# Optimization experiments

Measured on AMD Instinct MI355X. Metric: run time of the kernel, lower is better.

Reference implementation:

```python
import jax, jax.numpy as jnp
import numpy as np

N_NODES = 50000
N_EDGES = 800000
IN_CH = 128
HID = 128
N_GRAPHS = 512


def setup_inputs() -> dict:
    key = jax.random.key(0)
    ks = jax.random.split(key, 12)
    x = jax.random.normal(ks[0], (N_NODES, IN_CH), dtype=jnp.float32)
    edge_index = jax.random.randint(ks[1], (2, N_EDGES), 0, N_NODES, dtype=jnp.int64)
    batch = jnp.sort(jax.random.randint(ks[2], (N_NODES,), 0, N_GRAPHS, dtype=jnp.int64))
    s = 0.05
    params = {
        'W1l': jax.random.normal(ks[3], (HID, IN_CH), dtype=jnp.float32) * s,
        'W1r': jax.random.normal(ks[4], (HID, IN_CH), dtype=jnp.float32) * s,
        'b1': jax.random.normal(ks[5], (HID,), dtype=jnp.float32) * s,
        'W2l': jax.random.normal(ks[6], (HID, HID), dtype=jnp.float32) * s,
        'W2r': jax.random.normal(ks[7], (HID, HID), dtype=jnp.float32) * s,
        'b2': jax.random.normal(ks[8], (HID,), dtype=jnp.float32) * s,
        'W3l': jax.random.normal(ks[9], (HID, HID), dtype=jnp.float32) * s,
        'W3r': jax.random.normal(ks[10], (HID, HID), dtype=jnp.float32) * s,
        'b3': jax.random.normal(ks[11], (HID,), dtype=jnp.float32) * s,
    }
    return {'x': x, 'edge_index': edge_index, 'batch': batch, **params}


def reference(x, edge_index, batch, W1l, W1r, b1, W2l, W2r, b2, W3l, W3r, b3):
    src = edge_index[0]
    dst = edge_index[1]
    n = x.shape[0]
    # in-degree for mean aggregation (nodes with no in-edges get 0 aggregate)
    deg = jax.ops.segment_sum(jnp.ones((src.shape[0],), x.dtype), dst, num_segments=n)
    inv_deg = (1.0 / jnp.maximum(deg, 1.0))[:, None]  # [N,1]

    def sage(h, Wl, Wr, b):
        # gather neighbor feats, scatter-mean to targets, then linear + root term
        agg = jax.ops.segment_sum(h[src], dst, num_segments=n) * inv_deg  # [N,d]
        return agg @ Wl.T + h @ Wr.T + b

    h = jax.nn.relu(sage(x, W1l, W1r, b1))
    h = jax.nn.relu(sage(h, W2l, W2r, b2))
    h = jax.nn.relu(sage(h, W3l, W3r, b3))

    # global mean pool over graph ids
    counts = jax.ops.segment_sum(jnp.ones((n,), h.dtype), batch, num_segments=N_GRAPHS)
    pooled = jax.ops.segment_sum(h, batch, num_segments=N_GRAPHS)
    return pooled / jnp.maximum(counts, 1.0)[:, None]
```

## Files before the change

kernel.cpp:

```cpp
#include <hip/hip_runtime.h>

#define N_NODES 50000
#define NP 50048
#define N_EDGES 800000
#define N_GRAPHS 512
#define F 128
#define ELLW 64

#define CASTX_BLOCKS 3128
#define CASTW_BLOCKS 48
#define ZERO_BLOCKS 49

typedef __bf16 bf16x8 __attribute__((ext_vector_type(8)));
typedef float f32x4 __attribute__((ext_vector_type(4)));
typedef unsigned short ushort_t;
typedef unsigned int uint_t;

__device__ inline ushort_t f2bf(float f) {
    uint_t u = __float_as_uint(f);
    u += 0x7FFFu + ((u >> 16) & 1u);
    return (ushort_t)(u >> 16);
}
__device__ inline float bf2f(ushort_t u) {
    return __uint_as_float(((uint_t)u) << 16);
}
__device__ inline uint_t pack2(float a, float b) {
    return (uint_t)f2bf(a) | ((uint_t)f2bf(b) << 16);
}

__global__ __launch_bounds__(256) void k_prep(
    const float* __restrict__ x,
    const float* __restrict__ w0, const float* __restrict__ w1,
    const float* __restrict__ w2, const float* __restrict__ w3,
    const float* __restrict__ w4, const float* __restrict__ w5,
    ushort_t* __restrict__ X, ushort_t* __restrict__ WB,
    int* __restrict__ cnt) {
    int b = blockIdx.x;
    int t = threadIdx.x;
    if (b < CASTX_BLOCKS) {
        int i = (b * 256 + t) * 8;
        uint4 o = make_uint4(0, 0, 0, 0);
        if (i < N_NODES * F) {
            float4 v0 = *(const float4*)&x[i];
            float4 v1 = *(const float4*)&x[i + 4];
            o = make_uint4(pack2(v0.x, v0.y), pack2(v0.z, v0.w),
                           pack2(v1.x, v1.y), pack2(v1.z, v1.w));
        }
        *(uint4*)&X[i] = o;
    } else if (b < CASTX_BLOCKS + CASTW_BLOCKS) {
        int idx = (b - CASTX_BLOCKS) * 256 + t;
        int m = idx >> 11;
        int o = (idx & 2047) * 8;
        const float* src = w0;
        if (m == 1) src = w1; else if (m == 2) src = w2; else if (m == 3) src = w3;
        else if (m == 4) src = w4; else if (m == 5) src = w5;
        float4 v0 = *(const float4*)&src[o];
        float4 v1 = *(const float4*)&src[o + 4];
        *(uint4*)&WB[m * 16384 + o] =
            make_uint4(pack2(v0.x, v0.y), pack2(v0.z, v0.w),
                       pack2(v1.x, v1.y), pack2(v1.z, v1.w));
    } else {
        int i = ((b - CASTX_BLOCKS - CASTW_BLOCKS) * 256 + t) * 4;
        *(int4*)&cnt[i] = make_int4(0, 0, 0, 0);
    }
}

__global__ __launch_bounds__(256) void k_fillell(const int* __restrict__ src,
                                                 const int* __restrict__ dst,
                                                 int* __restrict__ cnt,
                                                 int* __restrict__ ell) {
    int e = blockIdx.x * 256 + threadIdx.x;
    if (e < N_EDGES) {
        int d = dst[e];
        int pos = atomicAdd(&cnt[d], 1);
        if (pos < ELLW) ell[(d << 6) + pos] = src[e];
    }
}

__device__ inline void addrow(float* a, uint4 v) {
    a[0] += __uint_as_float(v.x << 16); a[1] += __uint_as_float(v.x & 0xFFFF0000u);
    a[2] += __uint_as_float(v.y << 16); a[3] += __uint_as_float(v.y & 0xFFFF0000u);
    a[4] += __uint_as_float(v.z << 16); a[5] += __uint_as_float(v.z & 0xFFFF0000u);
    a[6] += __uint_as_float(v.w << 16); a[7] += __uint_as_float(v.w & 0xFFFF0000u);
}

__global__ __launch_bounds__(256) void k_gather(const ushort_t* __restrict__ h,
                                                const int* __restrict__ ell,
                                                const int* __restrict__ cnt,
                                                ushort_t* __restrict__ agg) {
    int t = blockIdx.x * 256 + threadIdx.x;
    int n = t >> 4;
    int lane = t & 15;
    if (n >= N_NODES) return;
    int deg = min(cnt[n], ELLW);
    const int* el = ell + (n << 6);
    const uint4* h4 = (const uint4*)h;
    float ax[8], ay[8];
#pragma unroll
    for (int j = 0; j < 8; j++) { ax[j] = 0.f; ay[j] = 0.f; }
    int i = 0;
    for (; i + 4 <= deg; i += 4) {
        int s0 = el[i], s1 = el[i + 1], s2 = el[i + 2], s3 = el[i + 3];
        uint4 v0 = h4[(size_t)s0 * 16 + lane];
        uint4 v1 = h4[(size_t)s1 * 16 + lane];
        uint4 v2 = h4[(size_t)s2 * 16 + lane];
        uint4 v3 = h4[(size_t)s3 * 16 + lane];
        addrow(ax, v0); addrow(ay, v1); addrow(ax, v2); addrow(ay, v3);
    }
    for (; i < deg; i++) {
        uint4 v0 = h4[(size_t)el[i] * 16 + lane];
        addrow(ax, v0);
    }
    float sc = 1.0f / fmaxf((float)deg, 1.0f);
    uint_t r[4];
#pragma unroll
    for (int j = 0; j < 4; j++)
        r[j] = pack2((ax[2 * j] + ay[2 * j]) * sc,
                     (ax[2 * j + 1] + ay[2 * j + 1]) * sc);
    ((uint4*)agg)[(size_t)n * 16 + lane] = make_uint4(r[0], r[1], r[2], r[3]);
}

__global__ __launch_bounds__(256) void k_linear(const ushort_t* __restrict__ agg,
                                                const ushort_t* h,
                                                const ushort_t* __restrict__ Wl,
                                                const ushort_t* __restrict__ Wr,
                                                const float* __restrict__ bias,
                                                ushort_t* out) {
    __shared__ uint4 Alds4[512];
    __shared__ uint4 Blds4[1024];
    ushort_t* Alds = (ushort_t*)Alds4;
    ushort_t* Blds = (ushort_t*)Blds4;

    int t = threadIdx.x;
    int w = t >> 6;
    int lane = t & 63;
    int bm = blockIdx.x * 64;
    int wm = (w & 1) * 32;
    int wn = (w >> 1) * 64;
    int lrow = lane & 15;
    int kg = lane >> 4;

    f32x4 acc[2][4];
#pragma unroll
    for (int i = 0; i < 2; i++)
#pragma unroll
        for (int j = 0; j < 4; j++) acc[i][j] = (f32x4){0.f, 0.f, 0.f, 0.f};

    for (int iter = 0; iter < 4; iter++) {
        int kk = iter * 64;
        const ushort_t* A = (kk < 128) ? agg : h;
        const ushort_t* W = (kk < 128) ? Wl : Wr;
        int k0 = kk & 127;

        __syncthreads();
#pragma unroll
        for (int p = 0; p < 2; p++) {
            int chunkA = p * 4 + w;
            const ushort_t* gA = A + (size_t)(bm + lane) * F + k0 + chunkA * 8;
            ushort_t* lA = Alds + (size_t)(chunkA * 64) * 8;
            __builtin_amdgcn_global_load_lds(
                (const __attribute__((address_space(1))) void*)gA,
                (__attribute__((address_space(3))) void*)lA, 16, 0, 0);
        }
#pragma unroll
        for (int p = 0; p < 4; p++) {
            int chunkB = p * 2 + (w >> 1);
            int rbase = (w & 1) * 64;
            const ushort_t* gB = W + (size_t)(rbase + lane) * F + k0 + chunkB * 8;
            ushort_t* lB = Blds + (size_t)(chunkB * 128 + rbase) * 8;
            __builtin_amdgcn_global_load_lds(
                (const __attribute__((address_space(1))) void*)gB,
                (__attribute__((address_space(3))) void*)lB, 16, 0, 0);
        }
        __syncthreads();

#pragma unroll
        for (int ks = 0; ks < 2; ks++) {
            bf16x8 af[2], bfr[4];
#pragma unroll
            for (int i = 0; i < 2; i++)
                af[i] = *(const bf16x8*)(Alds +
                    (size_t)((ks * 4 + kg) * 64 + wm + i * 16 + lrow) * 8);
#pragma unroll
            for (int j = 0; j < 4; j++)
                bfr[j] = *(const bf16x8*)(Blds +
                    (size_t)((ks * 4 + kg) * 128 + wn + j * 16 + lrow) * 8);
#pragma unroll
            for (int i = 0; i < 2; i++)
#pragma unroll
                for (int j = 0; j < 4; j++)
                    acc[i][j] = __builtin_amdgcn_mfma_f32_16x16x32_bf16(
                        af[i], bfr[j], acc[i][j], 0, 0, 0);
        }
    }

    int quad = lane >> 4;
#pragma unroll
    for (int j = 0; j < 4; j++) {
        int c = wn + j * 16 + lrow;
        float bj = bias[c];
#pragma unroll
        for (int i = 0; i < 2; i++) {
#pragma unroll
            for (int r = 0; r < 4; r++) {
                int row = bm + wm + i * 16 + quad * 4 + r;
                if (row < N_NODES) {
                    float v = fmaxf(acc[i][j][r] + bj, 0.0f);
                    out[(size_t)row * F + c] = f2bf(v);
                }
            }
        }
    }
}

__global__ __launch_bounds__(128) void k_pool(const ushort_t* __restrict__ h,
                                              const int* __restrict__ batch,
                                              float* __restrict__ out) {
    int g = blockIdx.x;
    int j = threadIdx.x;
    int lo = 0, hi = N_NODES;
    while (lo < hi) {
        int m = (lo + hi) >> 1;
        if (batch[m] < g) lo = m + 1; else hi = m;
    }
    int start = lo;
    lo = start; hi = N_NODES;
    while (lo < hi) {
        int m = (lo + hi) >> 1;
        if (batch[m] < g + 1) lo = m + 1; else hi = m;
    }
    int end = lo;
    float s = 0.0f;
    for (int n = start; n < end; n++) s += bf2f(h[(size_t)n * F + j]);
    out[g * F + j] = s / fmaxf((float)(end - start), 1.0f);
}

extern "C" void kernel_launch(void* const* d_in, const int* in_sizes, int n_in,
                              void* d_out, int out_size, void* d_ws, size_t ws_size,
                              hipStream_t stream) {
    const float* x   = (const float*)d_in[0];
    const int*   ei  = (const int*)d_in[1];
    const int* batch = (const int*)d_in[2];
    const float* W1l = (const float*)d_in[3];
    const float* W1r = (const float*)d_in[4];
    const float* b1  = (const float*)d_in[5];
    const float* W2l = (const float*)d_in[6];
    const float* W2r = (const float*)d_in[7];
    const float* b2  = (const float*)d_in[8];
    const float* W3l = (const float*)d_in[9];
    const float* W3r = (const float*)d_in[10];
    const float* b3  = (const float*)d_in[11];
    float* out = (float*)d_out;

    const int* src = ei;
    const int* dst = ei + N_EDGES;

    ushort_t* X   = (ushort_t*)d_ws;
    ushort_t* H   = X + (size_t)NP * F;
    ushort_t* AGG = H + (size_t)NP * F;
    ushort_t* WB  = AGG + (size_t)NP * F;
    int* cnt = (int*)(WB + 6 * 16384);
    int* ell = cnt + 50176;

    const ushort_t* Wb1l = WB;
    const ushort_t* Wb1r = WB + 16384;
    const ushort_t* Wb2l = WB + 2 * 16384;
    const ushort_t* Wb2r = WB + 3 * 16384;
    const ushort_t* Wb3l = WB + 4 * 16384;
    const ushort_t* Wb3r = WB + 5 * 16384;

    k_prep<<<CASTX_BLOCKS + CASTW_BLOCKS + ZERO_BLOCKS, 256, 0, stream>>>(
        x, W1l, W1r, W2l, W2r, W3l, W3r, X, WB, cnt);
    k_fillell<<<(N_EDGES + 255) / 256, 256, 0, stream>>>(src, dst, cnt, ell);

    const int gatherBlocks = (N_NODES * 16 + 255) / 256;
    const int linearBlocks = NP / 64;

    k_gather<<<gatherBlocks, 256, 0, stream>>>(X, ell, cnt, AGG);
    k_linear<<<linearBlocks, 256, 0, stream>>>(AGG, X, Wb1l, Wb1r, b1, H);
    k_gather<<<gatherBlocks, 256, 0, stream>>>(H, ell, cnt, AGG);
    k_linear<<<linearBlocks, 256, 0, stream>>>(AGG, H, Wb2l, Wb2r, b2, H);
    k_gather<<<gatherBlocks, 256, 0, stream>>>(H, ell, cnt, AGG);
    k_linear<<<linearBlocks, 256, 0, stream>>>(AGG, H, Wb3l, Wb3r, b3, H);

    k_pool<<<N_GRAPHS, 128, 0, stream>>>(H, batch, out);
}
```

Measured before the change: 329.9 us.

## Fuse ELL fill into prep kernel, store 16-bit neighbor indices, unroll gather by 8

After: 336.0 us. Within noise of the previous version (+1.8%).

```diff
diff --git a/kernel.cpp b/kernel.cpp
--- a/kernel.cpp
+++ b/kernel.cpp
@@ -7,9 +7,9 @@
 #define F 128
 #define ELLW 64
 
+#define FILL_BLOCKS 3125
 #define CASTX_BLOCKS 3128
 #define CASTW_BLOCKS 48
-#define ZERO_BLOCKS 49
 
 typedef __bf16 bf16x8 __attribute__((ext_vector_type(8)));
 typedef float f32x4 __attribute__((ext_vector_type(4)));
@@ -28,17 +28,23 @@
     return (uint_t)f2bf(a) | ((uint_t)f2bf(b) << 16);
 }
 
-__global__ __launch_bounds__(256) void k_prep(
+__global__ __launch_bounds__(256) void k_build(
     const float* __restrict__ x,
     const float* __restrict__ w0, const float* __restrict__ w1,
     const float* __restrict__ w2, const float* __restrict__ w3,
     const float* __restrict__ w4, const float* __restrict__ w5,
+    const int* __restrict__ src, const int* __restrict__ dst,
     ushort_t* __restrict__ X, ushort_t* __restrict__ WB,
-    int* __restrict__ cnt) {
+    int* __restrict__ cnt, ushort_t* __restrict__ ell) {
     int b = blockIdx.x;
     int t = threadIdx.x;
-    if (b < CASTX_BLOCKS) {
-        int i = (b * 256 + t) * 8;
+    if (b < FILL_BLOCKS) {
+        int e = b * 256 + t;
+        int d = dst[e];
+        int pos = atomicAdd(&cnt[d], 1);
+        if (pos < ELLW) ell[(d << 6) + pos] = (ushort_t)src[e];
+    } else if (b < FILL_BLOCKS + CASTX_BLOCKS) {
+        int i = ((b - FILL_BLOCKS) * 256 + t) * 8;
         uint4 o = make_uint4(0, 0, 0, 0);
         if (i < N_NODES * F) {
             float4 v0 = *(const float4*)&x[i];
@@ -47,33 +53,18 @@
                            pack2(v1.x, v1.y), pack2(v1.z, v1.w));
         }
         *(uint4*)&X[i] = o;
-    } else if (b < CASTX_BLOCKS + CASTW_BLOCKS) {
-        int idx = (b - CASTX_BLOCKS) * 256 + t;
+    } else {
+        int idx = (b - FILL_BLOCKS - CASTX_BLOCKS) * 256 + t;
         int m = idx >> 11;
         int o = (idx & 2047) * 8;
-        const float* src = w0;
-        if (m == 1) src = w1; else if (m == 2) src = w2; else if (m == 3) src = w3;
-        else if (m == 4) src = w4; else if (m == 5) src = w5;
-        float4 v0 = *(const float4*)&src[o];
-        float4 v1 = *(const float4*)&src[o + 4];
+        const float* s = w0;
+        if (m == 1) s = w1; else if (m == 2) s = w2; else if (m == 3) s = w3;
+        else if (m == 4) s = w4; else if (m == 5) s = w5;
+        float4 v0 = *(const float4*)&s[o];
+        float4 v1 = *(const float4*)&s[o + 4];
         *(uint4*)&WB[m * 16384 + o] =
             make_uint4(pack2(v0.x, v0.y), pack2(v0.z, v0.w),
                        pack2(v1.x, v1.y), pack2(v1.z, v1.w));
-    } else {
-        int i = ((b - CASTX_BLOCKS - CASTW_BLOCKS) * 256 + t) * 4;
-        *(int4*)&cnt[i] = make_int4(0, 0, 0, 0);
-    }
-}
-
-__global__ __launch_bounds__(256) void k_fillell(const int* __restrict__ src,
-                                                 const int* __restrict__ dst,
-                                                 int* __restrict__ cnt,
-                                                 int* __restrict__ ell) {
-    int e = blockIdx.x * 256 + threadIdx.x;
-    if (e < N_EDGES) {
-        int d = dst[e];
-        int pos = atomicAdd(&cnt[d], 1);
-        if (pos < ELLW) ell[(d << 6) + pos] = src[e];
     }
 }
 
@@ -85,7 +76,7 @@
 }
 
 __global__ __launch_bounds__(256) void k_gather(const ushort_t* __restrict__ h,
-                                                const int* __restrict__ ell,
+                                                const ushort_t* __restrict__ ell,
                                                 const int* __restrict__ cnt,
                                                 ushort_t* __restrict__ agg) {
     int t = blockIdx.x * 256 + threadIdx.x;
@@ -93,19 +84,28 @@
     int lane = t & 15;
     if (n >= N_NODES) return;
     int deg = min(cnt[n], ELLW);
-    const int* el = ell + (n << 6);
+    const ushort_t* el = ell + (n << 6);
     const uint4* h4 = (const uint4*)h;
     float ax[8], ay[8];
 #pragma unroll
     for (int j = 0; j < 8; j++) { ax[j] = 0.f; ay[j] = 0.f; }
     int i = 0;
-    for (; i + 4 <= deg; i += 4) {
-        int s0 = el[i], s1 = el[i + 1], s2 = el[i + 2], s3 = el[i + 3];
+    for (; i + 8 <= deg; i += 8) {
+        uint4 iv = *(const uint4*)&el[i];
+        int s0 = iv.x & 0xFFFF, s1 = iv.x >> 16;
+        int s2 = iv.y & 0xFFFF, s3 = iv.y >> 16;
+        int s4 = iv.z & 0xFFFF, s5 = iv.z >> 16;
+        int s6 = iv.w & 0xFFFF, s7 = iv.w >> 16;
         uint4 v0 = h4[(size_t)s0 * 16 + lane];
         uint4 v1 = h4[(size_t)s1 * 16 + lane];
         uint4 v2 = h4[(size_t)s2 * 16 + lane];
         uint4 v3 = h4[(size_t)s3 * 16 + lane];
+        uint4 v4 = h4[(size_t)s4 * 16 + lane];
+        uint4 v5 = h4[(size_t)s5 * 16 + lane];
+        uint4 v6 = h4[(size_t)s6 * 16 + lane];
+        uint4 v7 = h4[(size_t)s7 * 16 + lane];
         addrow(ax, v0); addrow(ay, v1); addrow(ax, v2); addrow(ay, v3);
+        addrow(ax, v4); addrow(ay, v5); addrow(ax, v6); addrow(ay, v7);
     }
     for (; i < deg; i++) {
         uint4 v0 = h4[(size_t)el[i] * 16 + lane];
@@ -260,7 +260,7 @@
     ushort_t* AGG = H + (size_t)NP * F;
     ushort_t* WB  = AGG + (size_t)NP * F;
     int* cnt = (int*)(WB + 6 * 16384);
-    int* ell = cnt + 50176;
+    ushort_t* ell = (ushort_t*)(cnt + 50176);
 
     const ushort_t* Wb1l = WB;
     const ushort_t* Wb1r = WB + 16384;
@@ -269,9 +269,9 @@
     const ushort_t* Wb3l = WB + 4 * 16384;
     const ushort_t* Wb3r = WB + 5 * 16384;
 
-    k_prep<<<CASTX_BLOCKS + CASTW_BLOCKS + ZERO_BLOCKS, 256, 0, stream>>>(
-        x, W1l, W1r, W2l, W2r, W3l, W3r, X, WB, cnt);
-    k_fillell<<<(N_EDGES + 255) / 256, 256, 0, stream>>>(src, dst, cnt, ell);
+    hipMemsetAsync(cnt, 0, 50176 * sizeof(int), stream);
+    k_build<<<FILL_BLOCKS + CASTX_BLOCKS + CASTW_BLOCKS, 256, 0, stream>>>(
+        x, W1l, W1r, W2l, W2r, W3l, W3r, src, dst, X, WB, cnt, ell);
 
     const int gatherBlocks = (N_NODES * 16 + 255) / 256;
     const int linearBlocks = NP / 64;
```
